# Kernel tuning notes

Hardware: AMD Instinct MI355X
Metric: run time of the kernel (lower is better)

## Reference

```python
import jax, jax.numpy as jnp
import numpy as np

N_HEAD = 16

def setup_inputs() -> dict:
    key = jax.random.key(0)
    k1, k2, k3 = jax.random.split(key, 3)
    B, T, C = 4, 2048, 1024
    x = jax.random.normal(k1, (B, T, C), dtype=jnp.float32)
    W_attn = jax.random.normal(k2, (C, 3 * C), dtype=jnp.float32) * (1.0 / np.sqrt(C))
    W_proj = jax.random.normal(k3, (C, C), dtype=jnp.float32) * (1.0 / np.sqrt(C))
    return {"x": x, "W_attn": W_attn, "W_proj": W_proj}

def reference(x, W_attn, W_proj):
    B, T, C = x.shape
    H = N_HEAD
    D = C // H  # head_dim
    qkv = x @ W_attn                      # (B, T, 3C)
    q, k, v = jnp.split(qkv, 3, axis=-1)
    # (B, T, C) -> (B, H, T, D)
    q = q.reshape(B, T, H, D).transpose(0, 2, 1, 3)
    k = k.reshape(B, T, H, D).transpose(0, 2, 1, 3)
    v = v.reshape(B, T, H, D).transpose(0, 2, 1, 3)
    scale = 1.0 / np.sqrt(D)
    att = jnp.einsum('bhqd,bhkd->bhqk', q, k) * scale  # (B, H, T, T)
    causal = jnp.tril(jnp.ones((T, T), dtype=bool))
    att = jnp.where(causal[None, None, :, :], att, -jnp.inf)
    att = jax.nn.softmax(att, axis=-1)
    y = jnp.einsum('bhqk,bhkd->bhqd', att, v)          # (B, H, T, D)
    y = y.transpose(0, 2, 1, 3).reshape(B, T, C)
    y = y @ W_proj
    return y
```

## Files before the change

### kernel.cpp

```cpp
#include <hip/hip_runtime.h>
#include <hip/hip_bf16.h>
#include <stdint.h>

typedef __attribute__((ext_vector_type(8))) __bf16 bf16x8;
typedef __attribute__((ext_vector_type(4))) __bf16 bf16x4;
typedef __attribute__((ext_vector_type(4))) float f32x4;

static __device__ __forceinline__ ushort f2bf(float f) {
  union { float f; uint32_t u; } v; v.f = f;
  uint32_t u = v.u;
  u += 0x7fffu + ((u >> 16) & 1u);
  return (ushort)(u >> 16);
}

static __device__ __forceinline__ void gl_lds16(const ushort* g, ushort* l) {
  __builtin_amdgcn_global_load_lds(
      (__attribute__((address_space(1))) unsigned int*)(g),
      (__attribute__((address_space(3))) unsigned int*)(l), 16, 0, 0);
}

__global__ __launch_bounds__(256) void cast_f32_bf16(
    const float* __restrict__ in, ushort* __restrict__ out, int n) {
  int i = (blockIdx.x * 256 + threadIdx.x) * 4;
  if (i >= n) return;
  float4 v = *(const float4*)&in[i];
  ushort4 o;
  o.x = f2bf(v.x); o.y = f2bf(v.y); o.z = f2bf(v.z); o.w = f2bf(v.w);
  *(ushort4*)&out[i] = o;
}

__global__ __launch_bounds__(256) void transpose_cast(
    const float* __restrict__ W, ushort* __restrict__ Wt, int K, int N) {
  __shared__ ushort tile[32][33];
  int n0 = blockIdx.x * 32, k0 = blockIdx.y * 32;
  int tx = threadIdx.x, ty = threadIdx.y;
  #pragma unroll
  for (int r = ty; r < 32; r += 8)
    tile[r][tx] = f2bf(W[(size_t)(k0 + r) * N + n0 + tx]);
  __syncthreads();
  #pragma unroll
  for (int r = ty; r < 32; r += 8)
    Wt[(size_t)(n0 + r) * K + k0 + tx] = tile[tx][r];
}

template <int MODE>
__global__ __launch_bounds__(256, 3) void gemm_bt(
    const ushort* __restrict__ A, const ushort* __restrict__ Bt,
    float* __restrict__ Cf, int M, int N, int K,
    ushort* __restrict__ Qo, ushort* __restrict__ Ko, ushort* __restrict__ Vo) {
  __shared__ ushort smem[24576];
  ushort(*As)[128][32] = (ushort(*)[128][32])(smem);
  ushort(*Bs)[128][32] = (ushort(*)[128][32])(smem + 12288);
  const int tid = threadIdx.x;
  const int lane = tid & 63;
  const int w = tid >> 6;
  const int wm = (w >> 1) * 64, wn = (w & 1) * 64;
  const int fid = blockIdx.x;
  const int c = fid & 7;
  const int local = fid >> 3;
  const int m0 = (c * 8 + (local & 7)) * 128;
  const int n0 = (local >> 3) * 128;
  const int lr = lane & 15, kg = lane >> 4;
  const int grow = w * 16 + (lane >> 2);
  const int gcol = (lane & 3) * 8;

  auto stage = [&](int buf, int t) {
    const int k0 = t << 5;
    gl_lds16(&A[(size_t)(m0 + grow) * K + k0 + gcol], &As[buf][w * 16][0]);
    gl_lds16(&A[(size_t)(m0 + 64 + grow) * K + k0 + gcol],
             &As[buf][64 + w * 16][0]);
    gl_lds16(&Bt[(size_t)(n0 + grow) * K + k0 + gcol], &Bs[buf][w * 16][0]);
    gl_lds16(&Bt[(size_t)(n0 + 64 + grow) * K + k0 + gcol],
             &Bs[buf][64 + w * 16][0]);
  };

  f32x4 zero = {0.f, 0.f, 0.f, 0.f};
  f32x4 acc[4][4];
  #pragma unroll
  for (int i = 0; i < 4; i++)
    #pragma unroll
    for (int j = 0; j < 4; j++) acc[i][j] = zero;

  const int nsteps = K >> 5;
  stage(0, 0);
  stage(1, 1);
  for (int t = 0; t < nsteps; t++) {
    if (t + 1 < nsteps)
      asm volatile("s_waitcnt vmcnt(4)" ::: "memory");
    else
      asm volatile("s_waitcnt vmcnt(0)" ::: "memory");
    __builtin_amdgcn_s_barrier();
    asm volatile("" ::: "memory");
    if (t + 2 < nsteps) stage((t + 2) % 3, t + 2);
    const ushort(*Ac)[32] = As[t % 3];
    const ushort(*Bc)[32] = Bs[t % 3];
    bf16x8 af[4], bfr[4];
    #pragma unroll
    for (int i = 0; i < 4; i++)
      af[i] = *(const bf16x8*)&Ac[wm + i * 16 + lr][kg * 8];
    #pragma unroll
    for (int j = 0; j < 4; j++)
      bfr[j] = *(const bf16x8*)&Bc[wn + j * 16 + lr][kg * 8];
    __builtin_amdgcn_s_setprio(1);
    #pragma unroll
    for (int i = 0; i < 4; i++)
      #pragma unroll
      for (int j = 0; j < 4; j++)
        acc[i][j] = __builtin_amdgcn_mfma_f32_16x16x32_bf16(af[i], bfr[j],
                                                            acc[i][j], 0, 0, 0);
    __builtin_amdgcn_s_setprio(0);
  }

  if (MODE == 2) {
    #pragma unroll
    for (int i = 0; i < 4; i++)
      #pragma unroll
      for (int j = 0; j < 4; j++)
        #pragma unroll
        for (int r = 0; r < 4; r++) {
          int mrow = m0 + wm + i * 16 + kg * 4 + r;
          int ncol = n0 + wn + j * 16 + lr;
          Cf[(size_t)mrow * N + ncol] = acc[i][j][r];
        }
  } else {
    __syncthreads();
    ushort* Ls = smem + w * (64 * 72);
    const int which = (n0 + wn) >> 10;
    const int bb = (m0 + wm) >> 11;
    const int hh = ((n0 + wn) & 1023) >> 6;
    const size_t bh = (size_t)(bb * 16 + hh);
    const int t0 = (m0 + wm) & 2047;
    #pragma unroll
    for (int i = 0; i < 4; i++) {
      #pragma unroll
      for (int j = 0; j < 4; j++) {
        #pragma unroll
        for (int r = 0; r < 4; r++) {
          const int ml = i * 16 + kg * 4 + r;
          const int nl = j * 16 + lr;
          float vv = acc[i][j][r];
          if (which == 0) vv *= 0.18033688011112042f;
          ushort bv = f2bf(vv);
          if (which == 2)
            Ls[nl * 72 + ml] = bv;
          else
            Ls[ml * 72 + nl] = bv;
        }
      }
    }
    const int rsub = lane >> 3, chk = lane & 7;
    #pragma unroll
    for (int it = 0; it < 8; it++) {
      const int ridx = it * 8 + rsub;
      bf16x8 v = *(const bf16x8*)&Ls[ridx * 72 + chk * 8];
      if (which == 0)
        *(bf16x8*)&Qo[(bh * 2048 + t0 + ridx) * 64 + chk * 8] = v;
      else if (which == 1)
        *(bf16x8*)&Ko[(bh * 2048 + t0 + ridx) * 64 + chk * 8] = v;
      else
        *(bf16x8*)&Vo[(bh * 64 + ridx) * 2048 + t0 + chk * 8] = v;
    }
  }
}

__global__ __launch_bounds__(256, 4) void attn_fwd(
    const ushort* __restrict__ Q, const ushort* __restrict__ Kc,
    const ushort* __restrict__ Vt, ushort* __restrict__ Y) {
  __shared__ ushort Ks[2][64][64];
  __shared__ ushort Vs[2][64][64];
  __shared__ ushort Ps[4][16][64];
  const int tid = threadIdx.x;
  const int lane = tid & 63, w = tid >> 6;
  const int lr = lane & 15, kg = lane >> 4;
  int blk = blockIdx.x;
  blk = (blk & 7) * 128 + (blk >> 3);
  const int pair = blk & 15;
  const int bh = blk >> 4;
  const ushort* Qp = Q + (size_t)bh * 2048 * 64;
  const ushort* Kp = Kc + (size_t)bh * 2048 * 64;
  const ushort* Vp = Vt + (size_t)bh * 64 * 2048;
  const int b = bh >> 4, h = bh & 15;
  const int swz = (lr & 14) << 3;
  char* PsB = (char*)&Ps[w][0][0];
  const int srow = lane >> 3, schunk = lane & 7;
  const int cs0 = (kg ^ (lr & 7)) << 3;
  const int cs1 = ((kg ^ 4) ^ (lr & 7)) << 3;
  f32x4 zero = {0.f, 0.f, 0.f, 0.f};

  auto stageKV = [&](int buf, int k0) {
    #pragma unroll
    for (int c = 0; c < 2; c++) {
      const int rbase = w * 16 + c * 8;
      const int r = rbase + srow;
      gl_lds16(&Kp[(size_t)(k0 + r) * 64 + ((schunk ^ (r & 7)) << 3)],
               &Ks[buf][rbase][0]);
      gl_lds16(&Vp[(size_t)r * 2048 + k0 + ((schunk ^ (r & 7)) << 3)],
               &Vs[buf][rbase][0]);
    }
  };

  for (int half = 0; half < 2; half++) {
    const int j = half ? (31 - pair) : pair;
    const int q0b = j << 6;
    const int qw0 = q0b + w * 16;
    bf16x8 qf0 = *(const bf16x8*)&Qp[(size_t)(qw0 + lr) * 64 + kg * 8];
    bf16x8 qf1 = *(const bf16x8*)&Qp[(size_t)(qw0 + lr) * 64 + 32 + kg * 8];
    f32x4 o[4];
    #pragma unroll
    for (int dt = 0; dt < 4; dt++) o[dt] = zero;
    float lsum = 0.f;

    stageKV(0, 0);
    __syncthreads();
    for (int k0 = 0; k0 <= q0b; k0 += 64) {
      const int cur = (k0 >> 6) & 1;
      if (k0 < q0b) stageKV(cur ^ 1, k0 + 64);

      f32x4 s[4];
      #pragma unroll
      for (int ct = 0; ct < 4; ct++) {
        bf16x8 kf0 = *(const bf16x8*)&Ks[cur][ct * 16 + lr][cs0];
        bf16x8 kf1 = *(const bf16x8*)&Ks[cur][ct * 16 + lr][cs1];
        f32x4 z = zero;
        z = __builtin_amdgcn_mfma_f32_16x16x32_bf16(kf0, qf0, z, 0, 0, 0);
        z = __builtin_amdgcn_mfma_f32_16x16x32_bf16(kf1, qf1, z, 0, 0, 0);
        s[ct] = z;
      }
      if (k0 == q0b) {
        const int qrow = qw0 + lr;
        #pragma unroll
        for (int ct = 0; ct < 4; ct++)
          #pragma unroll
          for (int r = 0; r < 4; r++) {
            int kj = k0 + ct * 16 + kg * 4 + r;
            s[ct][r] = (kj > qrow) ? -1e30f : s[ct][r];
          }
      }
      #pragma unroll
      for (int ct = 0; ct < 4; ct++) {
        float p0 = exp2f(s[ct][0]);
        float p1 = exp2f(s[ct][1]);
        float p2 = exp2f(s[ct][2]);
        float p3 = exp2f(s[ct][3]);
        lsum += (p0 + p1) + (p2 + p3);
        bf16x4 pk = {(__bf16)p0, (__bf16)p1, (__bf16)p2, (__bf16)p3};
        *(bf16x4*)(PsB + lr * 128 + ((ct * 32 + kg * 8) ^ swz)) = pk;
      }
      bf16x8 pa0 = *(const bf16x8*)(PsB + lr * 128 + ((kg * 16) ^ swz));
      bf16x8 pa1 = *(const bf16x8*)(PsB + lr * 128 + ((64 + kg * 16) ^ swz));
      #pragma unroll
      for (int dt = 0; dt < 4; dt++) {
        bf16x8 vf0 = *(const bf16x8*)&Vs[cur][dt * 16 + lr][cs0];
        bf16x8 vf1 = *(const bf16x8*)&Vs[cur][dt * 16 + lr][cs1];
        f32x4 t = o[dt];
        t = __builtin_amdgcn_mfma_f32_16x16x32_bf16(pa0, vf0, t, 0, 0, 0);
        t = __builtin_amdgcn_mfma_f32_16x16x32_bf16(pa1, vf1, t, 0, 0, 0);
        o[dt] = t;
      }
      __syncthreads();
    }

    lsum += __shfl_xor(lsum, 16);
    lsum += __shfl_xor(lsum, 32);
    float inv = 1.f / lsum;
    f32x4 ib;
    #pragma unroll
    for (int r = 0; r < 4; r++) ib[r] = __shfl(inv, kg * 4 + r);
    #pragma unroll
    for (int dt = 0; dt < 4; dt++) {
      #pragma unroll
      for (int r = 0; r < 4; r++) {
        size_t t = (size_t)qw0 + kg * 4 + r;
        Y[((size_t)b * 2048 + t) * 1024 + h * 64 + dt * 16 + lr] =
            f2bf(o[dt][r] * ib[r]);
      }
    }
  }
}

extern "C" void kernel_launch(void* const* d_in, const int* in_sizes, int n_in,
                              void* d_out, int out_size, void* d_ws,
                              size_t ws_size, hipStream_t stream) {
  const float* x = (const float*)d_in[0];
  const float* Wa = (const float*)d_in[1];
  const float* Wp = (const float*)d_in[2];
  float* out = (float*)d_out;

  char* ws = (char*)d_ws;
  size_t off = 0;
  auto carve = [&](size_t bytes) {
    void* p = ws + off;
    off += (bytes + 255) & ~(size_t)255;
    return p;
  };
  ushort* Xb = (ushort*)carve(8192ull * 1024 * 2);
  ushort* Wat = (ushort*)carve(3072ull * 1024 * 2);
  ushort* Wpt = (ushort*)carve(1024ull * 1024 * 2);
  ushort* Qh = (ushort*)carve(64ull * 2048 * 64 * 2);
  ushort* Kh = (ushort*)carve(64ull * 2048 * 64 * 2);
  ushort* Vt = (ushort*)carve(64ull * 64 * 2048 * 2);
  ushort* Yb = (ushort*)carve(8192ull * 1024 * 2);

  cast_f32_bf16<<<8192, 256, 0, stream>>>(x, Xb, 8192 * 1024);
  transpose_cast<<<dim3(96, 32), dim3(32, 8), 0, stream>>>(Wa, Wat, 1024, 3072);
  transpose_cast<<<dim3(32, 32), dim3(32, 8), 0, stream>>>(Wp, Wpt, 1024, 1024);
  gemm_bt<1><<<1536, 256, 0, stream>>>(Xb, Wat, nullptr, 8192, 3072, 1024, Qh,
                                       Kh, Vt);
  attn_fwd<<<1024, 256, 0, stream>>>(Qh, Kh, Vt, Yb);
  gemm_bt<2><<<512, 256, 0, stream>>>(Yb, Wpt, out, 8192, 1024, 1024, nullptr,
                                      nullptr, nullptr);
}
```

Before: 175.8 us.

## Enlarge attention query tile to 128 rows and swizzle GEMM LDS columns

The attention kernel now gives each block 128 query rows, with each wave handling two 16-row tiles. Each K/V tile loaded into LDS is therefore reused across twice as many queries, and the grid is halved to 512 blocks with causal pairing over 16 tiles. Separately, the GEMM applies an XOR swizzle to the LDS column chunks on both the global-to-LDS store and the fragment reads, to reduce bank conflicts. The costs are more registers and lower occupancy (launch bound 4 to 2), some extra masked work on the diagonal tile, and fewer blocks to balance the load.

```diff
diff --git a/kernel.cpp b/kernel.cpp
--- a/kernel.cpp
+++ b/kernel.cpp
@@ -62,7 +62,7 @@
   const int n0 = (local >> 3) * 128;
   const int lr = lane & 15, kg = lane >> 4;
   const int grow = w * 16 + (lane >> 2);
-  const int gcol = (lane & 3) * 8;
+  const int gcol = (((lane & 3) ^ (((lane >> 2) + (lane >> 4)) & 3)) << 3);
 
   auto stage = [&](int buf, int t) {
     const int k0 = t << 5;
@@ -80,6 +80,8 @@
   for (int i = 0; i < 4; i++)
     #pragma unroll
     for (int j = 0; j < 4; j++) acc[i][j] = zero;
+
+  const int csel = ((kg ^ (((lr & 3) + (lr >> 2)) & 3)) << 3);
 
   const int nsteps = K >> 5;
   stage(0, 0);
@@ -97,10 +99,10 @@
     bf16x8 af[4], bfr[4];
     #pragma unroll
     for (int i = 0; i < 4; i++)
-      af[i] = *(const bf16x8*)&Ac[wm + i * 16 + lr][kg * 8];
+      af[i] = *(const bf16x8*)&Ac[wm + i * 16 + lr][csel];
     #pragma unroll
     for (int j = 0; j < 4; j++)
-      bfr[j] = *(const bf16x8*)&Bc[wn + j * 16 + lr][kg * 8];
+      bfr[j] = *(const bf16x8*)&Bc[wn + j * 16 + lr][csel];
     __builtin_amdgcn_s_setprio(1);
     #pragma unroll
     for (int i = 0; i < 4; i++)
@@ -163,7 +165,7 @@
   }
 }
 
-__global__ __launch_bounds__(256, 4) void attn_fwd(
+__global__ __launch_bounds__(256, 2) void attn_fwd(
     const ushort* __restrict__ Q, const ushort* __restrict__ Kc,
     const ushort* __restrict__ Vt, ushort* __restrict__ Y) {
   __shared__ ushort Ks[2][64][64];
@@ -173,9 +175,9 @@
   const int lane = tid & 63, w = tid >> 6;
   const int lr = lane & 15, kg = lane >> 4;
   int blk = blockIdx.x;
-  blk = (blk & 7) * 128 + (blk >> 3);
-  const int pair = blk & 15;
-  const int bh = blk >> 4;
+  blk = (blk & 7) * 64 + (blk >> 3);
+  const int pair = blk & 7;
+  const int bh = blk >> 3;
   const ushort* Qp = Q + (size_t)bh * 2048 * 64;
   const ushort* Kp = Kc + (size_t)bh * 2048 * 64;
   const ushort* Vp = Vt + (size_t)bh * 64 * 2048;
@@ -189,8 +191,8 @@
 
   auto stageKV = [&](int buf, int k0) {
     #pragma unroll
-    for (int c = 0; c < 2; c++) {
-      const int rbase = w * 16 + c * 8;
+    for (int cc = 0; cc < 2; cc++) {
+      const int rbase = w * 16 + cc * 8;
       const int r = rbase + srow;
       gl_lds16(&Kp[(size_t)(k0 + r) * 64 + ((schunk ^ (r & 7)) << 3)],
                &Ks[buf][rbase][0]);
@@ -200,79 +202,109 @@
   };
 
   for (int half = 0; half < 2; half++) {
-    const int j = half ? (31 - pair) : pair;
-    const int q0b = j << 6;
-    const int qw0 = q0b + w * 16;
-    bf16x8 qf0 = *(const bf16x8*)&Qp[(size_t)(qw0 + lr) * 64 + kg * 8];
-    bf16x8 qf1 = *(const bf16x8*)&Qp[(size_t)(qw0 + lr) * 64 + 32 + kg * 8];
-    f32x4 o[4];
-    #pragma unroll
-    for (int dt = 0; dt < 4; dt++) o[dt] = zero;
-    float lsum = 0.f;
+    const int j = half ? (15 - pair) : pair;
+    const int q0b = j << 7;
+    const int qw0 = q0b + w * 32;
+    bf16x8 qf[2][2];
+    #pragma unroll
+    for (int rt = 0; rt < 2; rt++) {
+      qf[rt][0] =
+          *(const bf16x8*)&Qp[(size_t)(qw0 + rt * 16 + lr) * 64 + kg * 8];
+      qf[rt][1] =
+          *(const bf16x8*)&Qp[(size_t)(qw0 + rt * 16 + lr) * 64 + 32 + kg * 8];
+    }
+    f32x4 o[2][4];
+    #pragma unroll
+    for (int rt = 0; rt < 2; rt++)
+      #pragma unroll
+      for (int dt = 0; dt < 4; dt++) o[rt][dt] = zero;
+    float lsum[2] = {0.f, 0.f};
+    const int kmax = q0b + 64;
 
     stageKV(0, 0);
     __syncthreads();
-    for (int k0 = 0; k0 <= q0b; k0 += 64) {
+    for (int k0 = 0; k0 <= kmax; k0 += 64) {
       const int cur = (k0 >> 6) & 1;
-      if (k0 < q0b) stageKV(cur ^ 1, k0 + 64);
-
-      f32x4 s[4];
+      if (k0 < kmax) stageKV(cur ^ 1, k0 + 64);
+
+      bf16x8 kf0[4], kf1[4];
       #pragma unroll
       for (int ct = 0; ct < 4; ct++) {
-        bf16x8 kf0 = *(const bf16x8*)&Ks[cur][ct * 16 + lr][cs0];
-        bf16x8 kf1 = *(const bf16x8*)&Ks[cur][ct * 16 + lr][cs1];
-        f32x4 z = zero;
-        z = __builtin_amdgcn_mfma_f32_16x16x32_bf16(kf0, qf0, z, 0, 0, 0);
-        z = __builtin_amdgcn_mfma_f32_16x16x32_bf16(kf1, qf1, z, 0, 0, 0);
-        s[ct] = z;
-      }
-      if (k0 == q0b) {
-        const int qrow = qw0 + lr;
-        #pragma unroll
-        for (int ct = 0; ct < 4; ct++)
+        kf0[ct] = *(const bf16x8*)&Ks[cur][ct * 16 + lr][cs0];
+        kf1[ct] = *(const bf16x8*)&Ks[cur][ct * 16 + lr][cs1];
+      }
+      f32x4 s[2][4];
+      #pragma unroll
+      for (int rt = 0; rt < 2; rt++)
+        #pragma unroll
+        for (int ct = 0; ct < 4; ct++) {
+          f32x4 z = zero;
+          z = __builtin_amdgcn_mfma_f32_16x16x32_bf16(kf0[ct], qf[rt][0], z, 0,
+                                                      0, 0);
+          z = __builtin_amdgcn_mfma_f32_16x16x32_bf16(kf1[ct], qf[rt][1], z, 0,
+                                                      0, 0);
+          s[rt][ct] = z;
+        }
+      bf16x8 vf0[4], vf1[4];
+      #pragma unroll
+      for (int dt = 0; dt < 4; dt++) {
+        vf0[dt] = *(const bf16x8*)&Vs[cur][dt * 16 + lr][cs0];
+        vf1[dt] = *(const bf16x8*)&Vs[cur][dt * 16 + lr][cs1];
+      }
+      #pragma unroll
+      for (int rt = 0; rt < 2; rt++) {
+        if (k0 + 63 > qw0 + rt * 16) {
+          const int qrow = qw0 + rt * 16 + lr;
           #pragma unroll
-          for (int r = 0; r < 4; r++) {
-            int kj = k0 + ct * 16 + kg * 4 + r;
-            s[ct][r] = (kj > qrow) ? -1e30f : s[ct][r];
-          }
-      }
-      #pragma unroll
-      for (int ct = 0; ct < 4; ct++) {
-        float p0 = exp2f(s[ct][0]);
-        float p1 = exp2f(s[ct][1]);
-        float p2 = exp2f(s[ct][2]);
-        float p3 = exp2f(s[ct][3]);
-        lsum += (p0 + p1) + (p2 + p3);
-        bf16x4 pk = {(__bf16)p0, (__bf16)p1, (__bf16)p2, (__bf16)p3};
-        *(bf16x4*)(PsB + lr * 128 + ((ct * 32 + kg * 8) ^ swz)) = pk;
-      }
-      bf16x8 pa0 = *(const bf16x8*)(PsB + lr * 128 + ((kg * 16) ^ swz));
-      bf16x8 pa1 = *(const bf16x8*)(PsB + lr * 128 + ((64 + kg * 16) ^ swz));
+          for (int ct = 0; ct < 4; ct++)
+            #pragma unroll
+            for (int r = 0; r < 4; r++) {
+              int kj = k0 + ct * 16 + kg * 4 + r;
+              s[rt][ct][r] = (kj > qrow) ? -1e30f : s[rt][ct][r];
+            }
+        }
+        float ls = 0.f;
+        #pragma unroll
+        for (int ct = 0; ct < 4; ct++) {
+          float p0 = exp2f(s[rt][ct][0]);
+          float p1 = exp2f(s[rt][ct][1]);
+          float p2 = exp2f(s[rt][ct][2]);
+          float p3 = exp2f(s[rt][ct][3]);
+          ls += (p0 + p1) + (p2 + p3);
+          bf16x4 pk = {(__bf16)p0, (__bf16)p1, (__bf16)p2, (__bf16)p3};
+          *(bf16x4*)(PsB + lr * 128 + ((ct * 32 + kg * 8) ^ swz)) = pk;
+        }
+        lsum[rt] += ls;
+        bf16x8 pa0 = *(const bf16x8*)(PsB + lr * 128 + ((kg * 16) ^ swz));
+        bf16x8 pa1 = *(const bf16x8*)(PsB + lr * 128 + ((64 + kg * 16) ^ swz));
+        #pragma unroll
+        for (int dt = 0; dt < 4; dt++) {
+          f32x4 t = o[rt][dt];
+          t = __builtin_amdgcn_mfma_f32_16x16x32_bf16(pa0, vf0[dt], t, 0, 0, 0);
+          t = __builtin_amdgcn_mfma_f32_16x16x32_bf16(pa1, vf1[dt], t, 0, 0, 0);
+          o[rt][dt] = t;
+        }
+      }
+      __syncthreads();
+    }
+
+    #pragma unroll
+    for (int rt = 0; rt < 2; rt++) {
+      float ls = lsum[rt];
+      ls += __shfl_xor(ls, 16);
+      ls += __shfl_xor(ls, 32);
+      float inv = 1.f / ls;
+      f32x4 ib;
+      #pragma unroll
+      for (int r = 0; r < 4; r++) ib[r] = __shfl(inv, kg * 4 + r);
       #pragma unroll
       for (int dt = 0; dt < 4; dt++) {
-        bf16x8 vf0 = *(const bf16x8*)&Vs[cur][dt * 16 + lr][cs0];
-        bf16x8 vf1 = *(const bf16x8*)&Vs[cur][dt * 16 + lr][cs1];
-        f32x4 t = o[dt];
-        t = __builtin_amdgcn_mfma_f32_16x16x32_bf16(pa0, vf0, t, 0, 0, 0);
-        t = __builtin_amdgcn_mfma_f32_16x16x32_bf16(pa1, vf1, t, 0, 0, 0);
-        o[dt] = t;
-      }
-      __syncthreads();
-    }
-
-    lsum += __shfl_xor(lsum, 16);
-    lsum += __shfl_xor(lsum, 32);
-    float inv = 1.f / lsum;
-    f32x4 ib;
-    #pragma unroll
-    for (int r = 0; r < 4; r++) ib[r] = __shfl(inv, kg * 4 + r);
-    #pragma unroll
-    for (int dt = 0; dt < 4; dt++) {
-      #pragma unroll
-      for (int r = 0; r < 4; r++) {
-        size_t t = (size_t)qw0 + kg * 4 + r;
-        Y[((size_t)b * 2048 + t) * 1024 + h * 64 + dt * 16 + lr] =
-            f2bf(o[dt][r] * ib[r]);
+        #pragma unroll
+        for (int r = 0; r < 4; r++) {
+          size_t t = (size_t)qw0 + rt * 16 + kg * 4 + r;
+          Y[((size_t)b * 2048 + t) * 1024 + h * 64 + dt * 16 + lr] =
+              f2bf(o[rt][dt][r] * ib[r]);
+        }
       }
     }
   }
@@ -306,7 +338,7 @@
   transpose_cast<<<dim3(32, 32), dim3(32, 8), 0, stream>>>(Wp, Wpt, 1024, 1024);
   gemm_bt<1><<<1536, 256, 0, stream>>>(Xb, Wat, nullptr, 8192, 3072, 1024, Qh,
                                        Kh, Vt);
-  attn_fwd<<<1024, 256, 0, stream>>>(Qh, Kh, Vt, Yb);
+  attn_fwd<<<512, 256, 0, stream>>>(Qh, Kh, Vt, Yb);
   gemm_bt<2><<<512, 256, 0, stream>>>(Yb, Wpt, out, 8192, 1024, 1024, nullptr,
                                       nullptr, nullptr);
 }
```

New measurement: 178.6 us. No clear change (+1.6%).
